# Kernel tuning notes

Hardware: AMD Instinct MI355X
Metric: run time of the kernel (lower is better)

## Reference

```python
import jax, jax.numpy as jnp
import numpy as np

CUBIC_A = -0.75  # torch bicubic coefficient


def _cubic_weights(t):
    # torch get_cubic_upsample_coefficients, t in [0,1): weights for taps at -1,0,1,2
    A = CUBIC_A
    def c1(x):
        return ((A + 2.0) * x - (A + 3.0)) * x * x + 1.0
    def c2(x):
        return ((A * x - 5.0 * A) * x + 8.0 * A) * x - 4.0 * A
    return jnp.stack([c2(t + 1.0), c1(t), c1(1.0 - t), c2(2.0 - t)])  # [4, ...]


def geo_cyclic_pad(x, p):
    # GeoCyclicPadding: pole rows are flipped and shifted by half the longitudes,
    # longitude is padded cyclically.
    B, C, H, W = x.shape
    top = jnp.roll(jnp.flip(x[:, :, :p, :], axis=2), W // 2, axis=3)
    bot = jnp.roll(jnp.flip(x[:, :, H - p:, :], axis=2), W // 2, axis=3)
    x = jnp.concatenate([top, x, bot], axis=2)
    x = jnp.concatenate([x[:, :, :, -p:], x, x[:, :, :, :p]], axis=3)
    return x


def bicubic_grid_sample(img, gx, gy):
    # img: [N, Hp, Wp]; gx, gy: [N, Ho, Wo] normalized coords in [-1, 1]
    # torch grid_sample(mode='bicubic', align_corners=True, padding_mode='border')
    N, Hp, Wp = img.shape
    ix = (gx + 1.0) * 0.5 * (Wp - 1)
    iy = (gy + 1.0) * 0.5 * (Hp - 1)
    ix0 = jnp.floor(ix)
    iy0 = jnp.floor(iy)
    tx = ix - ix0
    ty = iy - iy0
    wx = _cubic_weights(tx)  # [4, N, Ho, Wo]
    wy = _cubic_weights(ty)  # [4, N, Ho, Wo]
    offs = jnp.arange(-1, 3, dtype=jnp.int32)[:, None, None, None]
    xs = jnp.clip(ix0.astype(jnp.int32)[None] + offs, 0, Wp - 1)  # [4,N,Ho,Wo] (border)
    ys = jnp.clip(iy0.astype(jnp.int32)[None] + offs, 0, Hp - 1)
    n = jnp.arange(N, dtype=jnp.int32)[None, None, :, None, None]
    vals = img[n, ys[:, None], xs[None, :]]  # [4, 4, N, Ho, Wo]
    return jnp.einsum('jnhw,inhw,jinhw->nhw', wy, wx, vals)


def reference(hidden_features, lat_grid, lon_grid, W_vel, b_vel, dt):
    B, C, H, W = hidden_features.shape
    two_pi = 2.0 * jnp.pi
    # velocity net (pointwise conv hidden_dim -> 2*hidden_dim)
    vel = jnp.einsum('bchw,oc->bohw', hidden_features, W_vel) + b_vel[None, :, None, None]
    vel = vel.reshape(B, 2, C, H, W)
    u, v = vel[:, 0], vel[:, 1]
    lon_prime = -u * dt
    lat_prime = -v * dt
    lat_p = lat_grid[:, None]  # [B,1,H,W] broadcasts over C
    lon_p = lon_grid[:, None]
    # rotated -> standard lat/lon
    slp, clp = jnp.sin(lat_prime), jnp.cos(lat_prime)
    slo, clo = jnp.sin(lon_prime), jnp.cos(lon_prime)
    sp, cp = jnp.sin(lat_p), jnp.cos(lat_p)
    sin_lat = slp * cp + clp * clo * sp
    lat = jnp.arcsin(jnp.clip(sin_lat, -1.0 + 1e-7, 1.0 - 1e-7))
    num = clp * slo
    den = clp * clo * cp - slp * sp
    lon = jnp.remainder(lon_p + jnp.arctan2(num, den) + two_pi, two_pi)
    min_lat, max_lat = jnp.min(lat_grid), jnp.max(lat_grid)
    min_lon, max_lon = jnp.min(lon_grid), jnp.max(lon_grid)
    gx = 2.0 * (lon - min_lon) / (max_lon - min_lon) - 1.0
    gy = 2.0 * (lat - min_lat) / (max_lat - min_lat) - 1.0
    # periodic wrap in longitude, pole reflection in latitude
    gx = jnp.remainder(gx + 1.0, 2.0) - 1.0
    left = gx <= 0.0
    outer = jnp.abs(gy) > 1.0
    gx = jnp.where(outer & left, gx + 1.0, gx)
    gx = jnp.where(outer & (~left), gx - 1.0, gx)
    gy = jnp.where(gy < -1.0, -(2.0 + gy), gy)
    gy = jnp.where(gy > 1.0, 2.0 - gy, gy)
    # pad and rescale grid to padded size (align_corners=True)
    padded = geo_cyclic_pad(hidden_features, 1)  # [B,C,H+2,W+2]
    Hp, Wp = H + 2, W + 2
    gx = gx * (W / Wp)
    gy = gy * (H / Hp)
    img = padded.reshape(B * C, Hp, Wp)
    out = bicubic_grid_sample(img, gx.reshape(B * C, H, W), gy.reshape(B * C, H, W))
    return out.reshape(B, C, H, W)


def setup_inputs() -> dict:
    key = jax.random.key(0)
    k1, k2 = jax.random.split(key, 2)
    B, C, H, W = 2, 64, 180, 360
    hidden_features = jax.random.normal(k1, (B, C, H, W), dtype=jnp.float32)
    lat = jnp.linspace(-jnp.pi / 2, jnp.pi / 2, H, dtype=jnp.float32)
    lon = jnp.arange(W, dtype=jnp.float32) * (2.0 * jnp.pi / W)
    lat_grid = jnp.broadcast_to(lat[:, None], (H, W))
    lon_grid = jnp.broadcast_to(lon[None, :], (H, W))
    lat_grid = jnp.broadcast_to(lat_grid[None], (B, H, W)).astype(jnp.float32)
    lon_grid = jnp.broadcast_to(lon_grid[None], (B, H, W)).astype(jnp.float32)
    W_vel = jax.random.normal(k2, (2 * C, C), dtype=jnp.float32) * 0.02
    b_vel = jnp.zeros((2 * C,), dtype=jnp.float32)
    return {"hidden_features": hidden_features, "lat_grid": lat_grid,
            "lon_grid": lon_grid, "W_vel": W_vel, "b_vel": b_vel, "dt": 1.0}
```

## Files before the change

kernel.cpp:

```cpp
#include <hip/hip_runtime.h>
#include <math.h>

constexpr int B_ = 2, C_ = 64, H_ = 180, W_ = 360;
constexpr int HW = H_ * W_;
constexpr int Hp = H_ + 2, Wp = W_ + 2;
constexpr int O_ = 2 * C_;

typedef float float4a __attribute__((ext_vector_type(4), aligned(4)));

__device__ __forceinline__ float frem(float x, float y) {
    return x - floorf(x / y) * y;
}
__device__ __forceinline__ float frem2(float x) {
    return x - floorf(x * 0.5f) * 2.0f;
}

__device__ __forceinline__ float cub1(float x) {
    return (1.25f * x - 2.25f) * x * x + 1.0f;
}
__device__ __forceinline__ float cub2(float x) {
    return ((-0.75f * x + 3.75f) * x - 6.0f) * x + 3.0f;
}

__device__ __forceinline__ float fetch_pad(const float* __restrict__ img, int y, int x) {
    int wc = x - 1;
    if (x == 0)      wc = W_ - 1;
    if (x == Wp - 1) wc = 0;
    int hh = y - 1;
    bool top = (y == 0), bot = (y == Hp - 1);
    if (top) hh = 0;
    if (bot) hh = H_ - 1;
    if (top || bot) { wc += W_ / 2; if (wc >= W_) wc -= W_; }
    return img[hh * W_ + wc];
}

struct Coord { float tx, ty; int jx, jy; };

__device__ __forceinline__ Coord compute_coord(
    float u, float v, float dt, float sp, float cp, float lon_p,
    float min_lat, float min_lon, float inv_dlat, float inv_dlon)
{
    const float two_pi = 6.28318530717958647f;
    const float sxw = (float)W_ / (float)Wp;
    const float syh = (float)H_ / (float)Hp;

    const float lon_pr = -u * dt;
    const float lat_pr = -v * dt;
    float slp, clp, slo, clo;
    __sincosf(lat_pr, &slp, &clp);
    __sincosf(lon_pr, &slo, &clo);
    float sin_lat = slp * cp + clp * clo * sp;
    sin_lat = fminf(fmaxf(sin_lat, -1.0f + 1e-7f), 1.0f - 1e-7f);
    const float lat = asinf(sin_lat);
    const float num = clp * slo;
    const float den = clp * clo * cp - slp * sp;
    const float lon = frem(lon_p + atan2f(num, den) + two_pi, two_pi);

    float gx = (lon - min_lon) * inv_dlon - 1.0f;
    float gy = (lat - min_lat) * inv_dlat - 1.0f;
    gx = frem2(gx + 1.0f) - 1.0f;
    const bool left  = (gx <= 0.0f);
    const bool outer = (fabsf(gy) > 1.0f);
    if (outer) gx += left ? 1.0f : -1.0f;
    if (gy < -1.0f)     gy = -(2.0f + gy);
    else if (gy > 1.0f) gy = 2.0f - gy;
    gx *= sxw;
    gy *= syh;

    const float ix = (gx + 1.0f) * 0.5f * (float)(Wp - 1);
    const float iy = (gy + 1.0f) * 0.5f * (float)(Hp - 1);
    const float fx0 = floorf(ix), fy0 = floorf(iy);
    Coord cr;
    cr.tx = ix - fx0; cr.ty = iy - fy0;
    cr.jx = (int)fx0; cr.jy = (int)fy0;
    return cr;
}

__device__ __forceinline__ bool is_interior(const Coord& cr) {
    return (cr.jx >= 2) & (cr.jx <= Wp - 4) & (cr.jy >= 2) & (cr.jy <= Hp - 4);
}

__device__ __forceinline__ float bicubic_reduce(const float* t, float tx, float ty) {
    const float wx0 = cub2(tx + 1.0f), wx1 = cub1(tx);
    const float wx2 = cub1(1.0f - tx), wx3 = cub2(2.0f - tx);
    const float wy0 = cub2(ty + 1.0f), wy1 = cub1(ty);
    const float wy2 = cub1(1.0f - ty), wy3 = cub2(2.0f - ty);
    const float r0 = fmaf(wx3, t[3],  fmaf(wx2, t[2],  fmaf(wx1, t[1],  wx0 * t[0])));
    const float r1 = fmaf(wx3, t[7],  fmaf(wx2, t[6],  fmaf(wx1, t[5],  wx0 * t[4])));
    const float r2 = fmaf(wx3, t[11], fmaf(wx2, t[10], fmaf(wx1, t[9],  wx0 * t[8])));
    const float r3 = fmaf(wx3, t[15], fmaf(wx2, t[14], fmaf(wx1, t[13], wx0 * t[12])));
    return fmaf(wy3, r3, fmaf(wy2, r2, fmaf(wy1, r1, wy0 * r0)));
}

__device__ __forceinline__ void taps_interior(const float* __restrict__ img,
                                              const Coord& cr, float* t) {
    const float* __restrict__ p = img + (cr.jy - 2) * W_ + (cr.jx - 2);
#pragma unroll
    for (int r = 0; r < 4; ++r) {
        const float4a row = *(const float4a*)(p + r * W_);
        t[r * 4 + 0] = row.x; t[r * 4 + 1] = row.y;
        t[r * 4 + 2] = row.z; t[r * 4 + 3] = row.w;
    }
}

__device__ __forceinline__ void taps_border(const float* __restrict__ img,
                                            const Coord& cr, float* t) {
    int xs[4], ys[4];
#pragma unroll
    for (int r = 0; r < 4; ++r) {
        xs[r] = min(max(cr.jx - 1 + r, 0), Wp - 1);
        ys[r] = min(max(cr.jy - 1 + r, 0), Hp - 1);
    }
#pragma unroll
    for (int r = 0; r < 4; ++r)
#pragma unroll
        for (int cc = 0; cc < 4; ++cc)
            t[r * 4 + cc] = fetch_pad(img, ys[r], xs[cc]);
}

__device__ __forceinline__ float advect_one(
    const float* __restrict__ img, float u, float v, float dt,
    float sp, float cp, float lon_p,
    float min_lat, float min_lon, float inv_dlat, float inv_dlon)
{
    const Coord cr = compute_coord(u, v, dt, sp, cp, lon_p,
                                   min_lat, min_lon, inv_dlat, inv_dlon);
    float t[16];
    if (__all(is_interior(cr))) taps_interior(img, cr, t);
    else                        taps_border(img, cr, t);
    return bicubic_reduce(t, cr.tx, cr.ty);
}

constexpr int P1_PXT = 256;
constexpr int P1_OG  = 2;
constexpr int P1_OPG = O_ / P1_OG;
constexpr int P1_TILES = (HW + P1_PXT - 1) / P1_PXT;

__global__ __launch_bounds__(P1_PXT, 4) void nsl_vel(
    const float* __restrict__ hidden, const float* __restrict__ W_vel,
    const float* __restrict__ b_vel, float* __restrict__ uv)
{
    const int bid  = blockIdx.x;
    const int tile = bid % P1_TILES;
    const int og   = (bid / P1_TILES) % P1_OG;
    const int b    = bid / (P1_TILES * P1_OG);
    const int px   = tile * P1_PXT + threadIdx.x;
    if (px >= HW) return;

    float acc[P1_OPG];
#pragma unroll
    for (int j = 0; j < P1_OPG; ++j) acc[j] = b_vel[og * P1_OPG + j];

    const float* hb = hidden + (size_t)b * C_ * HW + px;
    const float* Wg = W_vel + (size_t)og * P1_OPG * C_;

    float xf[4];
#pragma unroll
    for (int t = 0; t < 4; ++t) xf[t] = hb[(size_t)t * HW];

    for (int k0 = 0; k0 < C_; k0 += 4) {
        float xc[4];
#pragma unroll
        for (int t = 0; t < 4; ++t) xc[t] = xf[t];
        if (k0 + 4 < C_) {
#pragma unroll
            for (int t = 0; t < 4; ++t) xf[t] = hb[(size_t)(k0 + 4 + t) * HW];
        }
#pragma unroll
        for (int j = 0; j < P1_OPG; ++j) {
            const float* wr = Wg + (size_t)j * C_ + k0;
            acc[j] = fmaf(wr[0], xc[0], acc[j]);
            acc[j] = fmaf(wr[1], xc[1], acc[j]);
            acc[j] = fmaf(wr[2], xc[2], acc[j]);
            acc[j] = fmaf(wr[3], xc[3], acc[j]);
        }
    }

    float* o = uv + ((size_t)b * O_ + og * P1_OPG) * HW + px;
#pragma unroll
    for (int j = 0; j < P1_OPG; ++j) o[(size_t)j * HW] = acc[j];
}

constexpr int P2_TX = 16, P2_TY = 16;
constexpr int P2_GX = (W_ + P2_TX - 1) / P2_TX;
constexpr int P2_GY = (H_ + P2_TY - 1) / P2_TY;
constexpr int P2_NTILE = P2_GX * P2_GY;
constexpr int NXCD = 8;
constexpr int BC_PER_XCD = (B_ * C_) / NXCD;

__global__ __launch_bounds__(256, 8) void nsl_advect_x(
    const float* __restrict__ hidden,
    const float* __restrict__ lat_grid,
    const float* __restrict__ lon_grid,
    const float* __restrict__ uv,
    const float* __restrict__ dt_p,
    float* __restrict__ out)
{
    const int id   = blockIdx.x;
    const int xcd  = id & (NXCD - 1);
    const int slot = id >> 3;
    const int bcl  = slot / P2_NTILE;
    const int tile = slot - bcl * P2_NTILE;
    const int bc   = xcd * BC_PER_XCD + bcl;
    const int txx  = tile % P2_GX;
    const int tyy  = tile / P2_GX;

    const int lane = threadIdx.x & 63;
    const int wv   = threadIdx.x >> 6;
    const int lx   = lane & 15;
    const int ly   = (lane >> 4) + wv * 4;
    const int px   = txx * P2_TX + lx;
    const int py   = tyy * P2_TY + ly;
    if (px >= W_ || py >= H_) return;
    const int pix  = py * W_ + px;

    const int b  = bc >> 6;
    const int c  = bc & (C_ - 1);

    const float dt      = dt_p[0];
    const float min_lat = lat_grid[0];
    const float max_lat = lat_grid[(H_ - 1) * W_];
    const float min_lon = lon_grid[0];
    const float max_lon = lon_grid[W_ - 1];
    const float inv_dlat = 2.0f / (max_lat - min_lat);
    const float inv_dlon = 2.0f / (max_lon - min_lon);

    const float lat_p = lat_grid[(size_t)b * HW + pix];
    const float lon_p = lon_grid[(size_t)b * HW + pix];
    float sp, cp;
    __sincosf(lat_p, &sp, &cp);

    const float u = uv[((size_t)b * O_ + c) * HW + pix];
    const float v = uv[((size_t)b * O_ + C_ + c) * HW + pix];

    const float* __restrict__ img = hidden + (size_t)bc * HW;
    out[(size_t)bc * HW + pix] = advect_one(img, u, v, dt, sp, cp, lon_p,
                                            min_lat, min_lon, inv_dlat, inv_dlon);
}

constexpr int FB_CG = 4, FB_CPT = C_ / FB_CG, FB_PXT = 256;
constexpr int FB_TILES = (HW + FB_PXT - 1) / FB_PXT;

__global__ __launch_bounds__(FB_PXT, 6) void nsl_fused(
    const float* __restrict__ hidden, const float* __restrict__ lat_grid,
    const float* __restrict__ lon_grid, const float* __restrict__ W_vel,
    const float* __restrict__ b_vel, const float* __restrict__ dt_p,
    float* __restrict__ out)
{
    const int bid  = blockIdx.x;
    const int tile = bid % FB_TILES;
    const int cg   = (bid / FB_TILES) % FB_CG;
    const int b    = bid / (FB_TILES * FB_CG);
    const int px   = tile * FB_PXT + threadIdx.x;
    if (px >= HW) return;

    const float dt      = dt_p[0];
    const float min_lat = lat_grid[0];
    const float max_lat = lat_grid[(H_ - 1) * W_];
    const float min_lon = lon_grid[0];
    const float max_lon = lon_grid[W_ - 1];
    const float inv_dlat = 2.0f / (max_lat - min_lat);
    const float inv_dlon = 2.0f / (max_lon - min_lon);

    const float lat_p = lat_grid[(size_t)b * HW + px];
    const float lon_p = lon_grid[(size_t)b * HW + px];
    float sp, cp;
    __sincosf(lat_p, &sp, &cp);

    float u[FB_CPT], v[FB_CPT];
#pragma unroll
    for (int i = 0; i < FB_CPT; ++i) {
        u[i] = b_vel[cg * FB_CPT + i];
        v[i] = b_vel[C_ + cg * FB_CPT + i];
    }
    const float* hb = hidden + (size_t)b * C_ * HW + px;
#pragma unroll 2
    for (int k = 0; k < C_; ++k) {
        const float x = hb[(size_t)k * HW];
#pragma unroll
        for (int i = 0; i < FB_CPT; ++i) {
            u[i] = fmaf(W_vel[(size_t)(cg * FB_CPT + i) * C_ + k], x, u[i]);
            v[i] = fmaf(W_vel[(size_t)(C_ + cg * FB_CPT + i) * C_ + k], x, v[i]);
        }
    }

    for (int i = 0; i < FB_CPT; ++i) {
        const int c = cg * FB_CPT + i;
        const float* __restrict__ img = hidden + ((size_t)b * C_ + c) * HW;
        out[((size_t)b * C_ + c) * HW + px] =
            advect_one(img, u[i], v[i], dt, sp, cp, lon_p,
                       min_lat, min_lon, inv_dlat, inv_dlon);
    }
}

extern "C" void kernel_launch(void* const* d_in, const int* in_sizes, int n_in,
                              void* d_out, int out_size, void* d_ws, size_t ws_size,
                              hipStream_t stream) {
    const float* hidden   = (const float*)d_in[0];
    const float* lat_grid = (const float*)d_in[1];
    const float* lon_grid = (const float*)d_in[2];
    const float* W_vel    = (const float*)d_in[3];
    const float* b_vel    = (const float*)d_in[4];
    const float* dt_p     = (const float*)d_in[5];
    float* out = (float*)d_out;

    const size_t uv_bytes = (size_t)B_ * O_ * HW * sizeof(float);
    if (ws_size >= uv_bytes) {
        float* uv = (float*)d_ws;
        nsl_vel<<<B_ * P1_OG * P1_TILES, P1_PXT, 0, stream>>>(hidden, W_vel, b_vel, uv);
        const int grid2 = NXCD * BC_PER_XCD * P2_NTILE;
        nsl_advect_x<<<grid2, 256, 0, stream>>>(
            hidden, lat_grid, lon_grid, uv, dt_p, out);
    } else {
        nsl_fused<<<B_ * FB_CG * FB_TILES, FB_PXT, 0, stream>>>(
            hidden, lat_grid, lon_grid, W_vel, b_vel, dt_p, out);
    }
}
```

Before: 207.2 us.

## Split velocity conv into 4 output groups with XCD-aware tile mapping

The pointwise velocity conv now splits outputs into four groups of 32 instead of two of 64, which cuts accumulator registers and lets the launch bound allow 6 blocks per SIMD. Block IDs are remapped so that each of the 8 XCDs handles a contiguous range of pixel tiles, so the output groups that read the same hidden pixels share that XCD's L2. The channel loop double-buffers input loads in two 4-channel halves so loads overlap the FMAs. In exchange, each hidden pixel is read four times instead of twice, and the grid (8*32=256 tile slots vs 254 tiles) relies on an early-return guard.

Result: slower. 217.2 us (+4.9%).

```diff
diff --git a/kernel.cpp b/kernel.cpp
--- a/kernel.cpp
+++ b/kernel.cpp
@@ -132,18 +132,25 @@
 }
 
 constexpr int P1_PXT = 256;
-constexpr int P1_OG  = 2;
+constexpr int P1_OG  = 4;
 constexpr int P1_OPG = O_ / P1_OG;
 constexpr int P1_TILES = (HW + P1_PXT - 1) / P1_PXT;
-
-__global__ __launch_bounds__(P1_PXT, 4) void nsl_vel(
+constexpr int P1_NXCD = 8;
+constexpr int P1_TPX  = 32;
+
+__global__ __launch_bounds__(P1_PXT, 6) void nsl_vel4(
     const float* __restrict__ hidden, const float* __restrict__ W_vel,
     const float* __restrict__ b_vel, float* __restrict__ uv)
 {
-    const int bid  = blockIdx.x;
-    const int tile = bid % P1_TILES;
-    const int og   = (bid / P1_TILES) % P1_OG;
-    const int b    = bid / (P1_TILES * P1_OG);
+    const int id   = blockIdx.x;
+    const int xcd  = id & (P1_NXCD - 1);
+    const int slot = id >> 3;
+    const int lt   = slot & (P1_TPX - 1);
+    const int ogb  = slot >> 5;
+    const int og   = ogb & (P1_OG - 1);
+    const int b    = ogb >> 2;
+    const int tile = xcd * P1_TPX + lt;
+    if (tile >= P1_TILES) return;
     const int px   = tile * P1_PXT + threadIdx.x;
     if (px >= HW) return;
 
@@ -154,25 +161,36 @@
     const float* hb = hidden + (size_t)b * C_ * HW + px;
     const float* Wg = W_vel + (size_t)og * P1_OPG * C_;
 
-    float xf[4];
-#pragma unroll
-    for (int t = 0; t < 4; ++t) xf[t] = hb[(size_t)t * HW];
-
-    for (int k0 = 0; k0 < C_; k0 += 4) {
-        float xc[4];
-#pragma unroll
-        for (int t = 0; t < 4; ++t) xc[t] = xf[t];
-        if (k0 + 4 < C_) {
-#pragma unroll
-            for (int t = 0; t < 4; ++t) xf[t] = hb[(size_t)(k0 + 4 + t) * HW];
-        }
+    float xa[4], xb[4];
+#pragma unroll
+    for (int t = 0; t < 4; ++t) xa[t] = hb[(size_t)t * HW];
+#pragma unroll
+    for (int t = 0; t < 4; ++t) xb[t] = hb[(size_t)(4 + t) * HW];
+
+    for (int k0 = 0; k0 < C_; k0 += 8) {
 #pragma unroll
         for (int j = 0; j < P1_OPG; ++j) {
             const float* wr = Wg + (size_t)j * C_ + k0;
-            acc[j] = fmaf(wr[0], xc[0], acc[j]);
-            acc[j] = fmaf(wr[1], xc[1], acc[j]);
-            acc[j] = fmaf(wr[2], xc[2], acc[j]);
-            acc[j] = fmaf(wr[3], xc[3], acc[j]);
+            acc[j] = fmaf(wr[0], xa[0], acc[j]);
+            acc[j] = fmaf(wr[1], xa[1], acc[j]);
+            acc[j] = fmaf(wr[2], xa[2], acc[j]);
+            acc[j] = fmaf(wr[3], xa[3], acc[j]);
+        }
+        if (k0 + 8 < C_) {
+#pragma unroll
+            for (int t = 0; t < 4; ++t) xa[t] = hb[(size_t)(k0 + 8 + t) * HW];
+        }
+#pragma unroll
+        for (int j = 0; j < P1_OPG; ++j) {
+            const float* wr = Wg + (size_t)j * C_ + k0 + 4;
+            acc[j] = fmaf(wr[0], xb[0], acc[j]);
+            acc[j] = fmaf(wr[1], xb[1], acc[j]);
+            acc[j] = fmaf(wr[2], xb[2], acc[j]);
+            acc[j] = fmaf(wr[3], xb[3], acc[j]);
+        }
+        if (k0 + 12 < C_) {
+#pragma unroll
+            for (int t = 0; t < 4; ++t) xb[t] = hb[(size_t)(k0 + 12 + t) * HW];
         }
     }
 
@@ -307,7 +325,8 @@
     const size_t uv_bytes = (size_t)B_ * O_ * HW * sizeof(float);
     if (ws_size >= uv_bytes) {
         float* uv = (float*)d_ws;
-        nsl_vel<<<B_ * P1_OG * P1_TILES, P1_PXT, 0, stream>>>(hidden, W_vel, b_vel, uv);
+        const int grid1 = P1_NXCD * P1_TPX * P1_OG * B_;
+        nsl_vel4<<<grid1, P1_PXT, 0, stream>>>(hidden, W_vel, b_vel, uv);
         const int grid2 = NXCD * BC_PER_XCD * P2_NTILE;
         nsl_advect_x<<<grid2, 256, 0, stream>>>(
             hidden, lat_grid, lon_grid, uv, dt_p, out);
```

## Stage hidden features in LDS and compute all output channels per block

Applied to the files above, without the earlier changes.

The velocity kernel now loads each pixel's 64 input channels into shared memory once, then loops over 4 output groups of 32 channels each. Before, each of 2 output groups was a separate block that re-read the hidden tensor from global memory, so the input was read twice. This halves global reads of the hidden tensor at the cost of 32KB of LDS per 128-thread block, which limits occupancy, and a serial loop over output groups inside each block.

Measured after the change: 232.3 us. +12.1%, slower.

```diff
diff --git a/kernel.cpp b/kernel.cpp
--- a/kernel.cpp
+++ b/kernel.cpp
@@ -131,54 +131,56 @@
     return bicubic_reduce(t, cr.tx, cr.ty);
 }
 
-constexpr int P1_PXT = 256;
-constexpr int P1_OG  = 2;
-constexpr int P1_OPG = O_ / P1_OG;
-constexpr int P1_TILES = (HW + P1_PXT - 1) / P1_PXT;
-
-__global__ __launch_bounds__(P1_PXT, 4) void nsl_vel(
+constexpr int V2_PXB = 128;
+constexpr int V2_BPB = (HW + V2_PXB - 1) / V2_PXB;
+constexpr int V2_OG  = 4;
+constexpr int V2_OPG = O_ / V2_OG;
+
+__global__ __launch_bounds__(V2_PXB, 2) void nsl_vel_lds(
     const float* __restrict__ hidden, const float* __restrict__ W_vel,
     const float* __restrict__ b_vel, float* __restrict__ uv)
 {
-    const int bid  = blockIdx.x;
-    const int tile = bid % P1_TILES;
-    const int og   = (bid / P1_TILES) % P1_OG;
-    const int b    = bid / (P1_TILES * P1_OG);
-    const int px   = tile * P1_PXT + threadIdx.x;
-    if (px >= HW) return;
-
-    float acc[P1_OPG];
-#pragma unroll
-    for (int j = 0; j < P1_OPG; ++j) acc[j] = b_vel[og * P1_OPG + j];
+    __shared__ float xs[C_][V2_PXB];
+    const int id = blockIdx.x;
+    const int b  = id / V2_BPB;
+    const int t  = id - b * V2_BPB;
+    const int px = t * V2_PXB + threadIdx.x;
+    const bool ok = (px < HW);
 
     const float* hb = hidden + (size_t)b * C_ * HW + px;
-    const float* Wg = W_vel + (size_t)og * P1_OPG * C_;
-
-    float xf[4];
-#pragma unroll
-    for (int t = 0; t < 4; ++t) xf[t] = hb[(size_t)t * HW];
-
-    for (int k0 = 0; k0 < C_; k0 += 4) {
-        float xc[4];
-#pragma unroll
-        for (int t = 0; t < 4; ++t) xc[t] = xf[t];
-        if (k0 + 4 < C_) {
-#pragma unroll
-            for (int t = 0; t < 4; ++t) xf[t] = hb[(size_t)(k0 + 4 + t) * HW];
+    if (ok) {
+#pragma unroll 8
+        for (int k = 0; k < C_; ++k)
+            xs[k][threadIdx.x] = hb[(size_t)k * HW];
+    }
+    __syncthreads();
+    if (!ok) return;
+
+    float* ob = uv + (size_t)b * O_ * HW + px;
+#pragma unroll 1
+    for (int og = 0; og < V2_OG; ++og) {
+        const float* Wg = W_vel + (size_t)og * V2_OPG * C_;
+        float acc[V2_OPG];
+#pragma unroll
+        for (int j = 0; j < V2_OPG; ++j) acc[j] = b_vel[og * V2_OPG + j];
+
+        for (int k0 = 0; k0 < C_; k0 += 4) {
+            float xk[4];
+#pragma unroll
+            for (int q = 0; q < 4; ++q) xk[q] = xs[k0 + q][threadIdx.x];
+#pragma unroll
+            for (int j = 0; j < V2_OPG; ++j) {
+                const float* wr = Wg + (size_t)j * C_ + k0;
+                acc[j] = fmaf(wr[0], xk[0], acc[j]);
+                acc[j] = fmaf(wr[1], xk[1], acc[j]);
+                acc[j] = fmaf(wr[2], xk[2], acc[j]);
+                acc[j] = fmaf(wr[3], xk[3], acc[j]);
+            }
         }
 #pragma unroll
-        for (int j = 0; j < P1_OPG; ++j) {
-            const float* wr = Wg + (size_t)j * C_ + k0;
-            acc[j] = fmaf(wr[0], xc[0], acc[j]);
-            acc[j] = fmaf(wr[1], xc[1], acc[j]);
-            acc[j] = fmaf(wr[2], xc[2], acc[j]);
-            acc[j] = fmaf(wr[3], xc[3], acc[j]);
-        }
-    }
-
-    float* o = uv + ((size_t)b * O_ + og * P1_OPG) * HW + px;
-#pragma unroll
-    for (int j = 0; j < P1_OPG; ++j) o[(size_t)j * HW] = acc[j];
+        for (int j = 0; j < V2_OPG; ++j)
+            ob[(size_t)(og * V2_OPG + j) * HW] = acc[j];
+    }
 }
 
 constexpr int P2_TX = 16, P2_TY = 16;
@@ -307,7 +309,8 @@
     const size_t uv_bytes = (size_t)B_ * O_ * HW * sizeof(float);
     if (ws_size >= uv_bytes) {
         float* uv = (float*)d_ws;
-        nsl_vel<<<B_ * P1_OG * P1_TILES, P1_PXT, 0, stream>>>(hidden, W_vel, b_vel, uv);
+        const int grid1 = B_ * V2_BPB;
+        nsl_vel_lds<<<grid1, V2_PXB, 0, stream>>>(hidden, W_vel, b_vel, uv);
         const int grid2 = NXCD * BC_PER_XCD * P2_NTILE;
         nsl_advect_x<<<grid2, 256, 0, stream>>>(
             hidden, lat_grid, lon_grid, uv, dt_p, out);
```

## Fuse velocity projection into XCD-aware 2D-tiled advection kernel

Applied to the files above, without the earlier changes.

Replaces the two-kernel path (pointwise velocity conv written to workspace, then advection) with one fused kernel. Each 64-thread block covers a 16x4 pixel tile and computes u/v for 8 channels in registers, then advects those channels. Tiles are assigned per XCD so that neighbouring tiles and the channel groups that share the same hidden pixels land on the same L2. This removes the uv workspace round trip and one launch, but each pixel's 64-channel input is read 8 times (once per channel group), register pressure goes up, and blocks are small.

After: 278.8 us. +34.6%, slower.

```diff
diff --git a/kernel.cpp b/kernel.cpp
--- a/kernel.cpp
+++ b/kernel.cpp
@@ -131,163 +131,116 @@
     return bicubic_reduce(t, cr.tx, cr.ty);
 }
 
-constexpr int P1_PXT = 256;
-constexpr int P1_OG  = 2;
-constexpr int P1_OPG = O_ / P1_OG;
-constexpr int P1_TILES = (HW + P1_PXT - 1) / P1_PXT;
-
-__global__ __launch_bounds__(P1_PXT, 4) void nsl_vel(
-    const float* __restrict__ hidden, const float* __restrict__ W_vel,
-    const float* __restrict__ b_vel, float* __restrict__ uv)
-{
-    const int bid  = blockIdx.x;
-    const int tile = bid % P1_TILES;
-    const int og   = (bid / P1_TILES) % P1_OG;
-    const int b    = bid / (P1_TILES * P1_OG);
-    const int px   = tile * P1_PXT + threadIdx.x;
-    if (px >= HW) return;
-
-    float acc[P1_OPG];
-#pragma unroll
-    for (int j = 0; j < P1_OPG; ++j) acc[j] = b_vel[og * P1_OPG + j];
-
-    const float* hb = hidden + (size_t)b * C_ * HW + px;
-    const float* Wg = W_vel + (size_t)og * P1_OPG * C_;
-
-    float xf[4];
-#pragma unroll
-    for (int t = 0; t < 4; ++t) xf[t] = hb[(size_t)t * HW];
-
-    for (int k0 = 0; k0 < C_; k0 += 4) {
-        float xc[4];
-#pragma unroll
-        for (int t = 0; t < 4; ++t) xc[t] = xf[t];
-        if (k0 + 4 < C_) {
-#pragma unroll
-            for (int t = 0; t < 4; ++t) xf[t] = hb[(size_t)(k0 + 4 + t) * HW];
-        }
-#pragma unroll
-        for (int j = 0; j < P1_OPG; ++j) {
-            const float* wr = Wg + (size_t)j * C_ + k0;
-            acc[j] = fmaf(wr[0], xc[0], acc[j]);
-            acc[j] = fmaf(wr[1], xc[1], acc[j]);
-            acc[j] = fmaf(wr[2], xc[2], acc[j]);
-            acc[j] = fmaf(wr[3], xc[3], acc[j]);
-        }
-    }
-
-    float* o = uv + ((size_t)b * O_ + og * P1_OPG) * HW + px;
-#pragma unroll
-    for (int j = 0; j < P1_OPG; ++j) o[(size_t)j * HW] = acc[j];
-}
-
-constexpr int P2_TX = 16, P2_TY = 16;
-constexpr int P2_GX = (W_ + P2_TX - 1) / P2_TX;
-constexpr int P2_GY = (H_ + P2_TY - 1) / P2_TY;
-constexpr int P2_NTILE = P2_GX * P2_GY;
 constexpr int NXCD = 8;
-constexpr int BC_PER_XCD = (B_ * C_) / NXCD;
-
-__global__ __launch_bounds__(256, 8) void nsl_advect_x(
+constexpr int F2_TX = 16, F2_TY = 4;
+constexpr int F2_GX = (W_ + F2_TX - 1) / F2_TX;
+constexpr int F2_GY = (H_ + F2_TY - 1) / F2_TY;
+constexpr int F2_NTILE = F2_GX * F2_GY;
+constexpr int F2_CG  = 8;
+constexpr int F2_CPT = C_ / F2_CG;
+constexpr int F2_CGB = F2_CG * B_;
+constexpr int F2_TPX = (F2_NTILE + NXCD - 1) / NXCD;
+
+__global__ __launch_bounds__(64, 6) void nsl_fused_x(
     const float* __restrict__ hidden,
     const float* __restrict__ lat_grid,
     const float* __restrict__ lon_grid,
-    const float* __restrict__ uv,
+    const float* __restrict__ W_vel,
+    const float* __restrict__ b_vel,
     const float* __restrict__ dt_p,
     float* __restrict__ out)
 {
     const int id   = blockIdx.x;
     const int xcd  = id & (NXCD - 1);
     const int slot = id >> 3;
-    const int bcl  = slot / P2_NTILE;
-    const int tile = slot - bcl * P2_NTILE;
-    const int bc   = xcd * BC_PER_XCD + bcl;
-    const int txx  = tile % P2_GX;
-    const int tyy  = tile / P2_GX;
-
-    const int lane = threadIdx.x & 63;
-    const int wv   = threadIdx.x >> 6;
-    const int lx   = lane & 15;
-    const int ly   = (lane >> 4) + wv * 4;
-    const int px   = txx * P2_TX + lx;
-    const int py   = tyy * P2_TY + ly;
-    if (px >= W_ || py >= H_) return;
-    const int pix  = py * W_ + px;
-
-    const int b  = bc >> 6;
-    const int c  = bc & (C_ - 1);
+    const int cgb  = slot & (F2_CGB - 1);
+    const int lt   = slot >> 4;
+    const int tile = xcd * F2_TPX + lt;
+    if (tile >= F2_NTILE) return;
+    const int cg = cgb & (F2_CG - 1);
+    const int b  = cgb >> 3;
+
+    const int txx = tile % F2_GX;
+    const int tyy = tile / F2_GX;
+    const int lane = threadIdx.x;
+    const int lx = lane & 15;
+    const int ly = lane >> 4;
+    const int px = txx * F2_TX + lx;
+    const int py = tyy * F2_TY + ly;
+    if (px >= W_) return;
+    const int pix = py * W_ + px;
 
     const float dt      = dt_p[0];
     const float min_lat = lat_grid[0];
     const float max_lat = lat_grid[(H_ - 1) * W_];
     const float min_lon = lon_grid[0];
     const float max_lon = lon_grid[W_ - 1];
+    const float lat_p = lat_grid[(size_t)b * HW + pix];
+    const float lon_p = lon_grid[(size_t)b * HW + pix];
+
+    float u[F2_CPT], v[F2_CPT];
+#pragma unroll
+    for (int i = 0; i < F2_CPT; ++i) {
+        u[i] = b_vel[cg * F2_CPT + i];
+        v[i] = b_vel[C_ + cg * F2_CPT + i];
+    }
+    const float* hb = hidden + (size_t)b * C_ * HW + pix;
+    const float* Wu = W_vel + (size_t)(cg * F2_CPT) * C_;
+    const float* Wv = W_vel + (size_t)(C_ + cg * F2_CPT) * C_;
+
+    float xa[4], xb[4];
+#pragma unroll
+    for (int t = 0; t < 4; ++t) xa[t] = hb[(size_t)t * HW];
+#pragma unroll
+    for (int t = 0; t < 4; ++t) xb[t] = hb[(size_t)(4 + t) * HW];
+
+    for (int k0 = 0; k0 < C_; k0 += 8) {
+#pragma unroll
+        for (int j = 0; j < F2_CPT; ++j) {
+            const float* wru = Wu + (size_t)j * C_ + k0;
+            const float* wrv = Wv + (size_t)j * C_ + k0;
+            u[j] = fmaf(wru[0], xa[0], u[j]);
+            u[j] = fmaf(wru[1], xa[1], u[j]);
+            u[j] = fmaf(wru[2], xa[2], u[j]);
+            u[j] = fmaf(wru[3], xa[3], u[j]);
+            v[j] = fmaf(wrv[0], xa[0], v[j]);
+            v[j] = fmaf(wrv[1], xa[1], v[j]);
+            v[j] = fmaf(wrv[2], xa[2], v[j]);
+            v[j] = fmaf(wrv[3], xa[3], v[j]);
+        }
+        if (k0 + 8 < C_) {
+#pragma unroll
+            for (int t = 0; t < 4; ++t) xa[t] = hb[(size_t)(k0 + 8 + t) * HW];
+        }
+#pragma unroll
+        for (int j = 0; j < F2_CPT; ++j) {
+            const float* wru = Wu + (size_t)j * C_ + k0 + 4;
+            const float* wrv = Wv + (size_t)j * C_ + k0 + 4;
+            u[j] = fmaf(wru[0], xb[0], u[j]);
+            u[j] = fmaf(wru[1], xb[1], u[j]);
+            u[j] = fmaf(wru[2], xb[2], u[j]);
+            u[j] = fmaf(wru[3], xb[3], u[j]);
+            v[j] = fmaf(wrv[0], xb[0], v[j]);
+            v[j] = fmaf(wrv[1], xb[1], v[j]);
+            v[j] = fmaf(wrv[2], xb[2], v[j]);
+            v[j] = fmaf(wrv[3], xb[3], v[j]);
+        }
+        if (k0 + 12 < C_) {
+#pragma unroll
+            for (int t = 0; t < 4; ++t) xb[t] = hb[(size_t)(k0 + 12 + t) * HW];
+        }
+    }
+
     const float inv_dlat = 2.0f / (max_lat - min_lat);
     const float inv_dlon = 2.0f / (max_lon - min_lon);
-
-    const float lat_p = lat_grid[(size_t)b * HW + pix];
-    const float lon_p = lon_grid[(size_t)b * HW + pix];
     float sp, cp;
     __sincosf(lat_p, &sp, &cp);
 
-    const float u = uv[((size_t)b * O_ + c) * HW + pix];
-    const float v = uv[((size_t)b * O_ + C_ + c) * HW + pix];
-
-    const float* __restrict__ img = hidden + (size_t)bc * HW;
-    out[(size_t)bc * HW + pix] = advect_one(img, u, v, dt, sp, cp, lon_p,
-                                            min_lat, min_lon, inv_dlat, inv_dlon);
-}
-
-constexpr int FB_CG = 4, FB_CPT = C_ / FB_CG, FB_PXT = 256;
-constexpr int FB_TILES = (HW + FB_PXT - 1) / FB_PXT;
-
-__global__ __launch_bounds__(FB_PXT, 6) void nsl_fused(
-    const float* __restrict__ hidden, const float* __restrict__ lat_grid,
-    const float* __restrict__ lon_grid, const float* __restrict__ W_vel,
-    const float* __restrict__ b_vel, const float* __restrict__ dt_p,
-    float* __restrict__ out)
-{
-    const int bid  = blockIdx.x;
-    const int tile = bid % FB_TILES;
-    const int cg   = (bid / FB_TILES) % FB_CG;
-    const int b    = bid / (FB_TILES * FB_CG);
-    const int px   = tile * FB_PXT + threadIdx.x;
-    if (px >= HW) return;
-
-    const float dt      = dt_p[0];
-    const float min_lat = lat_grid[0];
-    const float max_lat = lat_grid[(H_ - 1) * W_];
-    const float min_lon = lon_grid[0];
-    const float max_lon = lon_grid[W_ - 1];
-    const float inv_dlat = 2.0f / (max_lat - min_lat);
-    const float inv_dlon = 2.0f / (max_lon - min_lon);
-
-    const float lat_p = lat_grid[(size_t)b * HW + px];
-    const float lon_p = lon_grid[(size_t)b * HW + px];
-    float sp, cp;
-    __sincosf(lat_p, &sp, &cp);
-
-    float u[FB_CPT], v[FB_CPT];
-#pragma unroll
-    for (int i = 0; i < FB_CPT; ++i) {
-        u[i] = b_vel[cg * FB_CPT + i];
-        v[i] = b_vel[C_ + cg * FB_CPT + i];
-    }
-    const float* hb = hidden + (size_t)b * C_ * HW + px;
-#pragma unroll 2
-    for (int k = 0; k < C_; ++k) {
-        const float x = hb[(size_t)k * HW];
-#pragma unroll
-        for (int i = 0; i < FB_CPT; ++i) {
-            u[i] = fmaf(W_vel[(size_t)(cg * FB_CPT + i) * C_ + k], x, u[i]);
-            v[i] = fmaf(W_vel[(size_t)(C_ + cg * FB_CPT + i) * C_ + k], x, v[i]);
-        }
-    }
-
-    for (int i = 0; i < FB_CPT; ++i) {
-        const int c = cg * FB_CPT + i;
+#pragma unroll 1
+    for (int i = 0; i < F2_CPT; ++i) {
+        const int c = cg * F2_CPT + i;
         const float* __restrict__ img = hidden + ((size_t)b * C_ + c) * HW;
-        out[((size_t)b * C_ + c) * HW + px] =
+        out[((size_t)b * C_ + c) * HW + pix] =
             advect_one(img, u[i], v[i], dt, sp, cp, lon_p,
                        min_lat, min_lon, inv_dlat, inv_dlon);
     }
@@ -304,15 +257,7 @@
     const float* dt_p     = (const float*)d_in[5];
     float* out = (float*)d_out;
 
-    const size_t uv_bytes = (size_t)B_ * O_ * HW * sizeof(float);
-    if (ws_size >= uv_bytes) {
-        float* uv = (float*)d_ws;
-        nsl_vel<<<B_ * P1_OG * P1_TILES, P1_PXT, 0, stream>>>(hidden, W_vel, b_vel, uv);
-        const int grid2 = NXCD * BC_PER_XCD * P2_NTILE;
-        nsl_advect_x<<<grid2, 256, 0, stream>>>(
-            hidden, lat_grid, lon_grid, uv, dt_p, out);
-    } else {
-        nsl_fused<<<B_ * FB_CG * FB_TILES, FB_PXT, 0, stream>>>(
-            hidden, lat_grid, lon_grid, W_vel, b_vel, dt_p, out);
-    }
-}
+    const int grid = NXCD * F2_TPX * F2_CGB;
+    nsl_fused_x<<<grid, 64, 0, stream>>>(
+        hidden, lat_grid, lon_grid, W_vel, b_vel, dt_p, out);
+}
```
